# Optimization experiments

Measured on AMD Instinct MI355X. Metric: run time of the kernel, lower is better.

Reference implementation:

```python
import jax, jax.numpy as jnp
import numpy as np

N = 200000
NNZ = 6400000
E = 500000
IN_P, IN_F, IN_N = 62, 37, 37
HID, LAT, DEC_HID = 256, 128, 64


def _p(key, shape, scale=0.05):
    return scale * jax.random.normal(key, shape, dtype=jnp.float32)


def setup_inputs() -> dict:
    key = jax.random.key(0)
    ks = jax.random.split(key, 32)
    inp = {
        'x_process': jax.random.normal(ks[0], (N, IN_P), dtype=jnp.float32),
        'x_file': jax.random.normal(ks[1], (N, IN_F), dtype=jnp.float32),
        'x_network': jax.random.normal(ks[2], (N, IN_N), dtype=jnp.float32),
        'adj_rows': jax.random.randint(ks[3], (NNZ,), 0, N, dtype=jnp.int32),
        'adj_cols': jax.random.randint(ks[4], (NNZ,), 0, N, dtype=jnp.int32),
        'adj_vals': jax.random.uniform(ks[5], (NNZ,), dtype=jnp.float32) / 32.0,
        'edge_src': jax.random.randint(ks[6], (E,), 0, N, dtype=jnp.int32),
        'edge_dst': jax.random.randint(ks[7], (E,), 0, N, dtype=jnp.int32),
        # per-view encoder params (weights stored [in, out])
        'Wp1': _p(ks[8], (IN_P, HID)), 'bp1': jnp.zeros((HID,), jnp.float32),
        'Wp2': _p(ks[9], (HID, LAT)), 'bp2': jnp.zeros((LAT,), jnp.float32),
        'Wf1': _p(ks[10], (IN_F, HID)), 'bf1': jnp.zeros((HID,), jnp.float32),
        'Wf2': _p(ks[11], (HID, LAT)), 'bf2': jnp.zeros((LAT,), jnp.float32),
        'Wn1': _p(ks[12], (IN_N, HID)), 'bn1': jnp.zeros((HID,), jnp.float32),
        'Wn2': _p(ks[13], (HID, LAT)), 'bn2': jnp.zeros((LAT,), jnp.float32),
        # gates
        'Wgp': _p(ks[14], (LAT, 1)), 'bgp': jnp.zeros((1,), jnp.float32),
        'Wgf': _p(ks[15], (LAT, 1)), 'bgf': jnp.zeros((1,), jnp.float32),
        'Wgn': _p(ks[16], (LAT, 1)), 'bgn': jnp.zeros((1,), jnp.float32),
        # mlp edge decoder
        'Wd1': _p(ks[17], (4 * LAT, DEC_HID)), 'bd1': jnp.zeros((DEC_HID,), jnp.float32),
        'Wd2': _p(ks[18], (DEC_HID, 1)), 'bd2': jnp.zeros((1,), jnp.float32),
    }
    return inp


def _spmm(rows, cols, vals, x):
    # sparse (COO) adjacency @ dense x : gather cols, scale, scatter-add into rows
    return jax.ops.segment_sum(vals[:, None] * x[cols], rows, num_segments=N)


def _encode_view(x, rows, cols, vals, W1, b1, W2, b2):
    h = jax.nn.relu(_spmm(rows, cols, vals, x) @ W1 + b1)  # dropout=0 / eval mode
    return _spmm(rows, cols, vals, h) @ W2 + b2


def reference(x_process, x_file, x_network, adj_rows, adj_cols, adj_vals,
              edge_src, edge_dst,
              Wp1, bp1, Wp2, bp2, Wf1, bf1, Wf2, bf2, Wn1, bn1, Wn2, bn2,
              Wgp, bgp, Wgf, bgf, Wgn, bgn, Wd1, bd1, Wd2, bd2):
    zp = _encode_view(x_process, adj_rows, adj_cols, adj_vals, Wp1, bp1, Wp2, bp2)
    zf = _encode_view(x_file, adj_rows, adj_cols, adj_vals, Wf1, bf1, Wf2, bf2)
    zn = _encode_view(x_network, adj_rows, adj_cols, adj_vals, Wn1, bn1, Wn2, bn2)
    # multi-view softmax gating -> fused latent [N, LAT]
    scores = jnp.concatenate([zp @ Wgp + bgp, zf @ Wgf + bgf, zn @ Wgn + bgn], axis=1)
    alpha = jax.nn.softmax(scores, axis=1)
    z = alpha[:, 0:1] * zp + alpha[:, 1:2] * zf + alpha[:, 2:3] * zn
    # mlp edge decoder: gather src/dst, concat features, small MLP
    zs, zd = z[edge_src], z[edge_dst]
    feats = jnp.concatenate([zs, zd, zs * zd, jnp.abs(zs - zd)], axis=1)  # [E, 4*LAT]
    logits = jax.nn.relu(feats @ Wd1 + bd1) @ Wd2 + bd2
    return logits[:, 0]
```

## Files before the change

kernel.cpp:

```cpp
#include <hip/hip_runtime.h>
#include <math.h>

#define Nn 200000
#define NNZV 6400000
#define NE 500000
#define HID 256
#define LAT 128

typedef _Float16 h2 __attribute__((ext_vector_type(2)));
typedef _Float16 f16x4 __attribute__((ext_vector_type(4)));
typedef _Float16 f16x8 __attribute__((ext_vector_type(8)));
typedef float f32x4 __attribute__((ext_vector_type(4)));
typedef short s16x8 __attribute__((ext_vector_type(8)));
struct alignas(8) H4 { _Float16 h[4]; };

__device__ __forceinline__ float rdlanef(float v, int k){
  return __uint_as_float(__builtin_amdgcn_readlane(__float_as_uint(v), k));
}

__global__ __launch_bounds__(256) void k_zero(int* __restrict__ cnt){
  int i = blockIdx.x*256 + threadIdx.x;
  if(i < Nn) cnt[i] = 0;
}

__global__ __launch_bounds__(256) void k_count(const int* __restrict__ rows, int* __restrict__ cnt){
  int i = blockIdx.x*256 + threadIdx.x;
  if(i < NNZV) atomicAdd(&cnt[rows[i]], 1);
}

__global__ __launch_bounds__(512) void k_scan_block(const int* __restrict__ cnt, int* __restrict__ incl, int* __restrict__ bsum){
  __shared__ int s[512];
  int t = threadIdx.x;
  int i = blockIdx.x*512 + t;
  int v = (i < Nn) ? cnt[i] : 0;
  s[t] = v; __syncthreads();
  for(int off = 1; off < 512; off <<= 1){
    int x = (t >= off) ? s[t-off] : 0;
    __syncthreads();
    s[t] += x;
    __syncthreads();
  }
  if(i < Nn) incl[i] = s[t];
  if(t == 511) bsum[blockIdx.x] = s[t];
}

__global__ __launch_bounds__(512) void k_scan_bsum(int* __restrict__ bsum, int nb){
  __shared__ int s[512];
  int t = threadIdx.x;
  int v = (t < nb) ? bsum[t] : 0;
  s[t] = v; __syncthreads();
  for(int off = 1; off < 512; off <<= 1){
    int x = (t >= off) ? s[t-off] : 0;
    __syncthreads();
    s[t] += x;
    __syncthreads();
  }
  if(t < nb) bsum[t] = s[t] - v;
}

__global__ __launch_bounds__(256) void k_finish(const int* __restrict__ incl, const int* __restrict__ boff,
                                                int* __restrict__ row_ptr, int* __restrict__ cur){
  int i = blockIdx.x*256 + threadIdx.x;
  if(i < Nn){
    int v = incl[i] + boff[i >> 9];
    row_ptr[i+1] = v;
    if(i < Nn-1) cur[i+1] = v;
  }
  if(i == 0){ row_ptr[0] = 0; cur[0] = 0; }
}

__global__ __launch_bounds__(256) void k_scatter(const int* __restrict__ rows, const int* __restrict__ cols,
    const float* __restrict__ vals, int* __restrict__ cur,
    int* __restrict__ cols_s, _Float16* __restrict__ vals_s){
  int i = blockIdx.x*256 + threadIdx.x;
  if(i >= NNZV) return;
  int r = rows[i];
  int j = atomicAdd(&cur[r], 1);
  cols_s[j] = cols[i];
  vals_s[j] = (_Float16)vals[i];
}

__global__ __launch_bounds__(256) void k_xpack(const float* __restrict__ xp, const float* __restrict__ xf,
    const float* __restrict__ xn, _Float16* __restrict__ xc0, _Float16* __restrict__ xtl){
  int idx = blockIdx.x*256 + threadIdx.x;
  int row = idx/18, c8 = idx - row*18;
  if(row >= Nn) return;
  H4 ha, hb;
  #pragma unroll
  for(int q = 0; q < 8; q++){
    int c = c8*8 + q;
    float x;
    if(c < 62)       x = xp[row*62 + c];
    else if(c < 99)  x = xf[row*37 + (c-62)];
    else if(c == 99) x = 0.f;
    else if(c < 137) x = xn[row*37 + (c-100)];
    else             x = 0.f;
    if(q < 4) ha.h[q] = (_Float16)x; else hb.h[q-4] = (_Float16)x;
  }
  if(c8 < 16){
    *(H4*)&xc0[(size_t)row*128 + c8*8]     = ha;
    *(H4*)&xc0[(size_t)row*128 + c8*8 + 4] = hb;
  } else {
    int t = (c8-16)*8;
    *(H4*)&xtl[(size_t)row*16 + t]     = ha;
    *(H4*)&xtl[(size_t)row*16 + t + 4] = hb;
  }
}

__global__ __launch_bounds__(256) void k_wpackF(
    const float* __restrict__ Wp1, const float* __restrict__ Wf1, const float* __restrict__ Wn1,
    const float* __restrict__ Wp2, const float* __restrict__ Wf2, const float* __restrict__ Wn2,
    _Float16* __restrict__ w1fp, _Float16* __restrict__ w1ff, _Float16* __restrict__ w1fn,
    _Float16* __restrict__ w2fp, _Float16* __restrict__ w2ff, _Float16* __restrict__ w2fn){
  int i = blockIdx.x*256 + threadIdx.x;
  if(i >= 18432) return;
  int v = i / 6144, rem = i - v*6144;
  const float* W1 = (v==0)?Wp1:((v==1)?Wf1:Wn1);
  const float* W2 = (v==0)?Wp2:((v==1)?Wf2:Wn2);
  _Float16* d1 = (v==0)?w1fp:((v==1)?w1ff:w1fn);
  _Float16* d2 = (v==0)?w2fp:((v==1)?w2ff:w2fn);
  int Kv = (v==0)?62:37;
  f16x8 o;
  if(rem < 2048){
    int kt = rem >> 10, r2 = rem & 1023;
    int nt = r2 >> 6, l = r2 & 63;
    int krow = kt*32 + (l>>4)*8, col = nt*16 + (l&15);
    #pragma unroll
    for(int j = 0; j < 8; j++){
      int k = krow + j;
      o[j] = (k < Kv) ? (_Float16)W1[k*256 + col] : (_Float16)0.f;
    }
    *(f16x8*)&d1[rem*8] = o;
  } else {
    int r = rem - 2048;
    int kt = r >> 9, nt = (r >> 6) & 7, l = r & 63;
    int krow = kt*32 + (l>>4)*8, col = nt*16 + (l&15);
    #pragma unroll
    for(int j = 0; j < 8; j++)
      o[j] = (_Float16)W2[(krow + j)*128 + col];
    *(f16x8*)&d2[r*8] = o;
  }
}

__global__ void k_wg2(const float* __restrict__ Wp2, const float* __restrict__ Wgp,
                      const float* __restrict__ Wf2, const float* __restrict__ Wgf,
                      const float* __restrict__ Wn2, const float* __restrict__ Wgn,
                      float* __restrict__ wg2){
  int k = threadIdx.x;
  float p = 0.f, f = 0.f, n = 0.f;
  for(int c = 0; c < 128; c++){
    p = fmaf(Wp2[k*128 + c], Wgp[c], p);
    f = fmaf(Wf2[k*128 + c], Wgf[c], f);
    n = fmaf(Wn2[k*128 + c], Wgn[c], n);
  }
  wg2[k] = p; wg2[256 + k] = f; wg2[512 + k] = n;
}

__global__ void k_const(const float* b2p, const float* Wgp, const float* bgp,
                        const float* b2f, const float* Wgf, const float* bgf,
                        const float* b2n, const float* Wgn, const float* bgn,
                        float* c3){
  int l = threadIdx.x;
  float p = 0.f, f = 0.f, n = 0.f;
  for(int j = l; j < LAT; j += 64){
    p += b2p[j]*Wgp[j];
    f += b2f[j]*Wgf[j];
    n += b2n[j]*Wgn[j];
  }
  #pragma unroll
  for(int off = 32; off >= 1; off >>= 1){
    p += __shfl_xor(p, off);
    f += __shfl_xor(f, off);
    n += __shfl_xor(n, off);
  }
  if(l == 0){ c3[0] = p + bgp[0]; c3[1] = f + bgf[0]; c3[2] = n + bgn[0]; }
}

__device__ __forceinline__ void encode_view(
    int tid, int row0, int voff, int Kv, int vidx,
    const _Float16 (*sT)[152], _Float16 (*sTv)[72], _Float16 (*hT)[264],
    const _Float16* __restrict__ w1frag, const float* __restrict__ b1,
    const _Float16* __restrict__ w2frag, const float* __restrict__ wg2v,
    _Float16* __restrict__ Y3, float* __restrict__ yg4f){
  int w = tid >> 6, l = tid & 63;
  int kg = l >> 4, er = l & 15;
  int mrow = (w & 1)*16 + er;

  {
    int row = tid >> 3, c0 = (tid & 7)*8;
    f16x8 vv;
    #pragma unroll
    for(int q = 0; q < 8; q++){
      int c = c0 + q;
      vv[q] = (c < Kv) ? sT[row][voff + c] : (_Float16)0.f;
    }
    *(f16x8*)&sTv[row][c0] = vv;
  }
  __syncthreads();

  {
    f16x8 a0 = *(const f16x8*)&sTv[mrow][kg*8];
    f16x8 a1 = *(const f16x8*)&sTv[mrow][32 + kg*8];
    int ntb = (w >> 1)*8;
    #pragma unroll
    for(int nt8 = 0; nt8 < 8; nt8++){
      int nt = ntb + nt8;
      f16x8 b0 = *(const f16x8*)&w1frag[(size_t)((0*16 + nt)*64 + l)*8];
      f16x8 b1v = *(const f16x8*)&w1frag[(size_t)((1*16 + nt)*64 + l)*8];
      f32x4 acc = {0.f, 0.f, 0.f, 0.f};
      acc = __builtin_amdgcn_mfma_f32_16x16x32_f16(a0, b0, acc, 0, 0, 0);
      acc = __builtin_amdgcn_mfma_f32_16x16x32_f16(a1, b1v, acc, 0, 0, 0);
      int col = nt*16 + er;
      float bb = b1[col];
      #pragma unroll
      for(int j = 0; j < 4; j++)
        hT[(w & 1)*16 + kg*4 + j][col] = (_Float16)fmaxf(acc[j] + bb, 0.f);
    }
  }
  __syncthreads();

  {
    int row = tid >> 3, cg = tid & 7;
    float p = 0.f;
    #pragma unroll 8
    for(int kk = 0; kk < 32; kk++)
      p = fmaf((float)hT[row][cg*32 + kk], wg2v[cg*32 + kk], p);
    p += __shfl_xor(p, 1);
    p += __shfl_xor(p, 2);
    p += __shfl_xor(p, 4);
    if((tid & 7) == 0) yg4f[(size_t)(row0 + row)*4 + vidx] = p;
  }

  {
    f16x8 af[8];
    #pragma unroll
    for(int kt = 0; kt < 8; kt++)
      af[kt] = *(const f16x8*)&hT[mrow][kt*32 + kg*8];
    __syncthreads();
    _Float16* yst = &hT[0][0];
    int ntb = (w >> 1)*4;
    #pragma unroll
    for(int nt4 = 0; nt4 < 4; nt4++){
      int nt = ntb + nt4;
      f32x4 acc = {0.f, 0.f, 0.f, 0.f};
      #pragma unroll
      for(int kt = 0; kt < 8; kt++){
        f16x8 bf = *(const f16x8*)&w2frag[(size_t)((kt*8 + nt)*64 + l)*8];
        acc = __builtin_amdgcn_mfma_f32_16x16x32_f16(af[kt], bf, acc, 0, 0, 0);
      }
      int col = nt*16 + er;
      #pragma unroll
      for(int j = 0; j < 4; j++)
        yst[((w & 1)*16 + kg*4 + j)*132 + col] = (_Float16)acc[j];
    }
    __syncthreads();
    int row = tid >> 3, c0 = (tid & 7)*16;
    f16x8 y0 = *(const f16x8*)&yst[row*132 + c0];
    f16x8 y1 = *(const f16x8*)&yst[row*132 + c0 + 8];
    _Float16* yo = &Y3[(size_t)(row0 + row)*384 + vidx*128 + c0];
    *(f16x8*)yo       = y0;
    *(f16x8*)(yo + 8) = y1;
  }
  __syncthreads();
}

__global__ __launch_bounds__(256, 5) void k_encfused(
    const int* __restrict__ row_ptr, const int* __restrict__ cols_s, const _Float16* __restrict__ vals_s,
    const _Float16* __restrict__ xc0, const _Float16* __restrict__ xtl,
    const _Float16* __restrict__ w1fp, const float* __restrict__ bp1, const _Float16* __restrict__ w2fp,
    const _Float16* __restrict__ w1ff, const float* __restrict__ bf1, const _Float16* __restrict__ w2ff,
    const _Float16* __restrict__ w1fn, const float* __restrict__ bn1, const _Float16* __restrict__ w2fn,
    const float* __restrict__ wg2,
    _Float16* __restrict__ Y3, float* __restrict__ yg4f){
  __shared__ _Float16 sT[32][152];
  __shared__ _Float16 sTv[32][72];
  __shared__ _Float16 hT[32][264];
  int tid = threadIdx.x;
  int lane = tid & 63, wid = tid >> 6;
  int hl = lane & 31;
  int half = lane >> 5;
  int base = lane & 32;
  int row0 = blockIdx.x * 32;
  bool hast = (hl < 4);
  const char* xc0b = (const char*)xc0;
  const char* xtlb = (const char*)xtl;

  for(int p = 0; p < 4; p++){
    int rr = wid*8 + p*2 + half;
    int r = row0 + rr;
    int start = row_ptr[r], end = row_ptr[r+1];
    int len = end - start;
    int lenO = __shfl(len, lane ^ 32);
    int lenmax = len > lenO ? len : lenO;
    float a0 = 0.f, a1 = 0.f, a2 = 0.f, a3 = 0.f;
    float t0 = 0.f, t1 = 0.f, t2 = 0.f, t3 = 0.f;
    for(int j0 = 0; j0 < lenmax; j0 += 32){
      int m = len - j0; if(m > 32) m = 32; if(m < 0) m = 0;
      int mO = lenO - j0; if(mO > 32) mO = 32; if(mO < 0) mO = 0;
      int mmax = m > mO ? m : mO;
      int mycol = 0; float myval = 0.f;
      if(hl < m){
        mycol = cols_s[start + j0 + hl];
        myval = (float)vals_s[start + j0 + hl];
      }
      int mpad = (mmax + 3) & ~3;
      for(int k = 0; k < mpad; k += 4){
        #pragma unroll
        for(int q = 0; q < 4; q++){
          int c = __shfl(mycol, base + k + q);
          float v = __shfl(myval, base + k + q);
          f16x4 xa = *(const f16x4*)(xc0b + (((unsigned)c) << 8) + hl*8);
          a0 = fmaf((float)xa[0], v, a0);
          a1 = fmaf((float)xa[1], v, a1);
          a2 = fmaf((float)xa[2], v, a2);
          a3 = fmaf((float)xa[3], v, a3);
          if(hast){
            f16x4 xb = *(const f16x4*)(xtlb + ((unsigned)c)*32u + hl*8);
            t0 = fmaf((float)xb[0], v, t0);
            t1 = fmaf((float)xb[1], v, t1);
            t2 = fmaf((float)xb[2], v, t2);
            t3 = fmaf((float)xb[3], v, t3);
          }
        }
      }
    }
    h2 s01; s01[0] = (_Float16)a0; s01[1] = (_Float16)a1;
    h2 s23; s23[0] = (_Float16)a2; s23[1] = (_Float16)a3;
    *(h2*)&sT[rr][4*hl]     = s01;
    *(h2*)&sT[rr][4*hl + 2] = s23;
    if(hast){
      h2 u01; u01[0] = (_Float16)t0; u01[1] = (_Float16)t1;
      h2 u23; u23[0] = (_Float16)t2; u23[1] = (_Float16)t3;
      *(h2*)&sT[rr][128 + 4*hl]     = u01;
      *(h2*)&sT[rr][128 + 4*hl + 2] = u23;
    }
  }
  __syncthreads();

  encode_view(tid, row0, 0,   62, 0, sT, sTv, hT, w1fp, bp1, w2fp, wg2,       Y3, yg4f);
  encode_view(tid, row0, 62,  37, 1, sT, sTv, hT, w1ff, bf1, w2ff, wg2 + 256, Y3, yg4f);
  encode_view(tid, row0, 100, 37, 2, sT, sTv, hT, w1fn, bn1, w2fn, wg2 + 512, Y3, yg4f);
}

__global__ __launch_bounds__(256, 8) void k_spmm2f(
    const int* __restrict__ row_ptr, const int* __restrict__ cols_s, const _Float16* __restrict__ vals_s,
    const _Float16* __restrict__ Y3,
    const float4* __restrict__ yg4, const float* __restrict__ c3,
    const float* __restrict__ b2p, const float* __restrict__ b2f, const float* __restrict__ b2n,
    _Float16* __restrict__ z){
  int tid = threadIdx.x;
  int lane = tid & 63;
  int hl = lane & 31;
  int half = lane >> 5;
  int base = lane & 32;
  int r = blockIdx.x*8 + (tid >> 6)*2 + half;
  int start = row_ptr[r], end = row_ptr[r+1];
  int len = end - start;
  int lenO = __shfl(len, lane ^ 32);
  int lenmax = len > lenO ? len : lenO;
  unsigned lo = hl*8;
  float ap0=0.f, ap1=0.f, ap2=0.f, ap3=0.f;
  float af0=0.f, af1=0.f, af2=0.f, af3=0.f;
  float an0=0.f, an1=0.f, an2=0.f, an3=0.f;
  float scp=0.f, scf=0.f, scn=0.f;
  const char* Yb = (const char*)Y3;
  for(int j0 = 0; j0 < lenmax; j0 += 32){
    int m = len - j0; if(m > 32) m = 32; if(m < 0) m = 0;
    int mO = lenO - j0; if(mO > 32) mO = 32; if(mO < 0) mO = 0;
    int mmax = m > mO ? m : mO;
    int mycol = 0; float myval = 0.f;
    if(hl < m){
      mycol = cols_s[start + j0 + hl];
      myval = (float)vals_s[start + j0 + hl];
      float4 g = yg4[mycol];
      scp = fmaf(myval, g.x, scp);
      scf = fmaf(myval, g.y, scf);
      scn = fmaf(myval, g.z, scn);
    }
    int mpad = (mmax + 3) & ~3;
    for(int k = 0; k < mpad; k += 4){
      #pragma unroll
      for(int q = 0; q < 4; q++){
        int c = __shfl(mycol, base + k + q);
        float v = __shfl(myval, base + k + q);
        const char* p = Yb + ((unsigned)c)*768u + lo;
        f16x4 yp = *(const f16x4*)(p);
        f16x4 yf = *(const f16x4*)(p + 256);
        f16x4 yn = *(const f16x4*)(p + 512);
        ap0 = fmaf((float)yp[0], v, ap0); ap1 = fmaf((float)yp[1], v, ap1);
        ap2 = fmaf((float)yp[2], v, ap2); ap3 = fmaf((float)yp[3], v, ap3);
        af0 = fmaf((float)yf[0], v, af0); af1 = fmaf((float)yf[1], v, af1);
        af2 = fmaf((float)yf[2], v, af2); af3 = fmaf((float)yf[3], v, af3);
        an0 = fmaf((float)yn[0], v, an0); an1 = fmaf((float)yn[1], v, an1);
        an2 = fmaf((float)yn[2], v, an2); an3 = fmaf((float)yn[3], v, an3);
      }
    }
  }
  #pragma unroll
  for(int off = 16; off >= 1; off >>= 1){
    scp += __shfl_xor(scp, off);
    scf += __shfl_xor(scf, off);
    scn += __shfl_xor(scn, off);
  }
  float sp = scp + c3[0], sf = scf + c3[1], sn = scn + c3[2];
  float mx = fmaxf(sp, fmaxf(sf, sn));
  float ep = expf(sp - mx), ef = expf(sf - mx), en = expf(sn - mx);
  float inv = 1.f / (ep + ef + en);
  float A0 = ep*inv, A1 = ef*inv, A2 = en*inv;
  int o = hl*4;
  float4 bp = *(const float4*)&b2p[o];
  float4 bf = *(const float4*)&b2f[o];
  float4 bn = *(const float4*)&b2n[o];
  H4 uz;
  uz.h[0] = (_Float16)(A0*(ap0 + bp.x) + A1*(af0 + bf.x) + A2*(an0 + bn.x));
  uz.h[1] = (_Float16)(A0*(ap1 + bp.y) + A1*(af1 + bf.y) + A2*(an1 + bn.y));
  uz.h[2] = (_Float16)(A0*(ap2 + bp.z) + A1*(af2 + bf.z) + A2*(an2 + bn.z));
  uz.h[3] = (_Float16)(A0*(ap3 + bp.w) + A1*(af3 + bf.w) + A2*(an3 + bn.w));
  *(H4*)&z[(size_t)r*LAT + o] = uz;
}

#define DEC_TILES (NE/16)
__global__ __launch_bounds__(256) void k_dec(
    const _Float16* __restrict__ z, const int* __restrict__ esrc, const int* __restrict__ edst,
    const float* __restrict__ Wd1, const float* __restrict__ bd1,
    const float* __restrict__ Wd2, const float* __restrict__ bd2, float* __restrict__ out){
  __shared__ float part[4][16][68];
  int tid = threadIdx.x;
  int w  = tid >> 6;
  int l  = tid & 63;
  int erow = l & 15;
  int kg   = l >> 4;

  f16x8 bfr[4][4];
  #pragma unroll
  for(int kt = 0; kt < 4; kt++){
    #pragma unroll
    for(int nt = 0; nt < 4; nt++){
      f16x8 bb;
      #pragma unroll
      for(int j = 0; j < 8; j++)
        bb[j] = (_Float16)Wd1[(w*128 + kt*32 + kg*8 + j)*64 + nt*16 + erow];
      bfr[kt][nt] = bb;
    }
  }

  int n0 = (tid & 15) * 4;
  int e2 = tid >> 4;
  float4 bb1 = *(const float4*)&bd1[n0];
  float4 w2v = *(const float4*)&Wd2[n0];
  float bias2 = bd2[0];

  for(int tile = blockIdx.x; tile < DEC_TILES; tile += gridDim.x){
    int e = tile*16 + erow;
    int si = esrc[e], di = edst[e];
    const f16x8* zs = (const f16x8*)&z[(size_t)si*LAT];
    const f16x8* zd = (const f16x8*)&z[(size_t)di*LAT];
    f16x8 afr[4];
    if(w == 0){
      #pragma unroll
      for(int kt = 0; kt < 4; kt++) afr[kt] = zs[kt*4 + kg];
    } else if(w == 1){
      #pragma unroll
      for(int kt = 0; kt < 4; kt++) afr[kt] = zd[kt*4 + kg];
    } else if(w == 2){
      #pragma unroll
      for(int kt = 0; kt < 4; kt++) afr[kt] = zs[kt*4 + kg] * zd[kt*4 + kg];
    } else {
      #pragma unroll
      for(int kt = 0; kt < 4; kt++){
        f16x8 d = zs[kt*4 + kg] - zd[kt*4 + kg];
        s16x8 m = __builtin_bit_cast(s16x8, d) & (short)0x7fff;
        afr[kt] = __builtin_bit_cast(f16x8, m);
      }
    }
    f32x4 zero = {0.f, 0.f, 0.f, 0.f};
    f32x4 acc[4] = {zero, zero, zero, zero};
    #pragma unroll
    for(int kt = 0; kt < 4; kt++){
      #pragma unroll
      for(int nt = 0; nt < 4; nt++)
        acc[nt] = __builtin_amdgcn_mfma_f32_16x16x32_f16(afr[kt], bfr[kt][nt], acc[nt], 0, 0, 0);
    }
    #pragma unroll
    for(int nt = 0; nt < 4; nt++){
      #pragma unroll
      for(int j = 0; j < 4; j++)
        part[w][kg*4 + j][nt*16 + erow] = acc[nt][j];
    }
    __syncthreads();
    float s0 = part[0][e2][n0+0] + part[1][e2][n0+0] + part[2][e2][n0+0] + part[3][e2][n0+0];
    float s1 = part[0][e2][n0+1] + part[1][e2][n0+1] + part[2][e2][n0+1] + part[3][e2][n0+1];
    float s2 = part[0][e2][n0+2] + part[1][e2][n0+2] + part[2][e2][n0+2] + part[3][e2][n0+2];
    float s3 = part[0][e2][n0+3] + part[1][e2][n0+3] + part[2][e2][n0+3] + part[3][e2][n0+3];
    float p = fmaxf(s0 + bb1.x, 0.f)*w2v.x + fmaxf(s1 + bb1.y, 0.f)*w2v.y
            + fmaxf(s2 + bb1.z, 0.f)*w2v.z + fmaxf(s3 + bb1.w, 0.f)*w2v.w;
    #pragma unroll
    for(int off = 1; off < 16; off <<= 1) p += __shfl_xor(p, off);
    if((tid & 15) == 0) out[tile*16 + e2] = p + bias2;
    __syncthreads();
  }
}

extern "C" void kernel_launch(void* const* d_in, const int* in_sizes, int n_in,
                              void* d_out, int out_size, void* d_ws, size_t ws_size,
                              hipStream_t stream) {
  const float* xp  = (const float*)d_in[0];
  const float* xf  = (const float*)d_in[1];
  const float* xn  = (const float*)d_in[2];
  const int* arows = (const int*)d_in[3];
  const int* acols = (const int*)d_in[4];
  const float* avals = (const float*)d_in[5];
  const int* esrc  = (const int*)d_in[6];
  const int* edst  = (const int*)d_in[7];
  const float* Wp1 = (const float*)d_in[8];  const float* bp1 = (const float*)d_in[9];
  const float* Wp2 = (const float*)d_in[10]; const float* bp2 = (const float*)d_in[11];
  const float* Wf1 = (const float*)d_in[12]; const float* bf1 = (const float*)d_in[13];
  const float* Wf2 = (const float*)d_in[14]; const float* bf2w = (const float*)d_in[15];
  const float* Wn1 = (const float*)d_in[16]; const float* bn1 = (const float*)d_in[17];
  const float* Wn2 = (const float*)d_in[18]; const float* bn2 = (const float*)d_in[19];
  const float* Wgp = (const float*)d_in[20]; const float* bgp = (const float*)d_in[21];
  const float* Wgf = (const float*)d_in[22]; const float* bgf = (const float*)d_in[23];
  const float* Wgn = (const float*)d_in[24]; const float* bgn = (const float*)d_in[25];
  const float* Wd1 = (const float*)d_in[26]; const float* bd1 = (const float*)d_in[27];
  const float* Wd2 = (const float*)d_in[28]; const float* bd2 = (const float*)d_in[29];
  float* out = (float*)d_out;
  (void)in_sizes; (void)n_in; (void)out_size; (void)ws_size;

  char* base = (char*)d_ws;
  size_t off = 0;
  auto alloc = [&](size_t nbytes) -> char* {
    off = (off + 255) & ~(size_t)255;
    char* p = base + off;
    off += nbytes;
    return p;
  };
  int*      row_ptr = (int*)     alloc((size_t)(Nn + 1) * 4);
  int*      cols_s  = (int*)     alloc((size_t)NNZV * 4);
  _Float16* vals_s  = (_Float16*)alloc((size_t)NNZV * 2);
  _Float16* xcat0   = (_Float16*)alloc((size_t)Nn * 128 * 2);
  _Float16* xtail   = (_Float16*)alloc((size_t)Nn * 16 * 2);
  _Float16* Y3      = (_Float16*)alloc((size_t)Nn * 384 * 2);
  float*    yg4     = (float*)   alloc((size_t)Nn * 4 * 4);
  float*    c3      = (float*)   alloc(256);
  float*    wg2     = (float*)   alloc(3 * 256 * 4);
  _Float16* w1fp = (_Float16*)alloc(16384*2);
  _Float16* w1ff = (_Float16*)alloc(16384*2);
  _Float16* w1fn = (_Float16*)alloc(16384*2);
  _Float16* w2fp = (_Float16*)alloc(32768*2);
  _Float16* w2ff = (_Float16*)alloc(32768*2);
  _Float16* w2fn = (_Float16*)alloc(32768*2);
  _Float16* z = xcat0;
  int* cur  = (int*)((char*)xcat0);
  int* incl = (int*)((char*)xcat0 + 1000000);
  int* bsum = (int*)((char*)xcat0 + 2000000);

  int NB = (Nn + 511) / 512;

  k_zero   <<<(Nn + 255)/256, 256, 0, stream>>>(cur);
  k_count  <<<(NNZV + 255)/256, 256, 0, stream>>>(arows, cur);
  k_scan_block<<<NB, 512, 0, stream>>>(cur, incl, bsum);
  k_scan_bsum<<<1, 512, 0, stream>>>(bsum, NB);
  k_finish <<<(Nn + 255)/256, 256, 0, stream>>>(incl, bsum, row_ptr, cur);
  k_scatter<<<(NNZV + 255)/256, 256, 0, stream>>>(arows, acols, avals, cur, cols_s, vals_s);

  k_xpack<<<(Nn*18 + 255)/256, 256, 0, stream>>>(xp, xf, xn, xcat0, xtail);
  k_wpackF<<<72, 256, 0, stream>>>(Wp1, Wf1, Wn1, Wp2, Wf2, Wn2,
                                   w1fp, w1ff, w1fn, w2fp, w2ff, w2fn);
  k_wg2<<<1, 256, 0, stream>>>(Wp2, Wgp, Wf2, Wgf, Wn2, Wgn, wg2);
  k_const<<<1, 64, 0, stream>>>(bp2, Wgp, bgp, bf2w, Wgf, bgf, bn2, Wgn, bgn, c3);

  k_encfused<<<Nn/32, 256, 0, stream>>>(row_ptr, cols_s, vals_s, xcat0, xtail,
      w1fp, bp1, w2fp,  w1ff, bf1, w2ff,  w1fn, bn1, w2fn,  wg2,
      Y3, yg4);

  k_spmm2f<<<Nn/8, 256, 0, stream>>>(row_ptr, cols_s, vals_s, Y3,
      (const float4*)yg4, c3, bp2, bf2w, bn2, z);

  k_dec<<<2048, 256, 0, stream>>>(z, esrc, edst, Wd1, bd1, Wd2, bd2, out);
}
```

Baseline: 2.308 ms.

## Split second SpMM into score kernel and two column-half gather passes

Moves the gating-score accumulation and softmax out of the second SpMM into a separate k_score kernel that writes per-row alpha into the reused xtail buffer. The SpMM itself is split into two launches, each handling half of the 128 latent columns with 4-byte loads per view, so each pass touches a smaller slice of Y3 and may get better cache locality from the random column gathers. In exchange, the CSR indices and values are read three times, there are extra launches, and each gather is narrower per lane.

Result: no change. 2.296 ms (-0.5%).

```diff
diff --git a/kernel.cpp b/kernel.cpp
--- a/kernel.cpp
+++ b/kernel.cpp
@@ -13,10 +13,6 @@
 typedef float f32x4 __attribute__((ext_vector_type(4)));
 typedef short s16x8 __attribute__((ext_vector_type(8)));
 struct alignas(8) H4 { _Float16 h[4]; };
-
-__device__ __forceinline__ float rdlanef(float v, int k){
-  return __uint_as_float(__builtin_amdgcn_readlane(__float_as_uint(v), k));
-}
 
 __global__ __launch_bounds__(256) void k_zero(int* __restrict__ cnt){
   int i = blockIdx.x*256 + threadIdx.x;
@@ -342,10 +338,45 @@
   encode_view(tid, row0, 100, 37, 2, sT, sTv, hT, w1fn, bn1, w2fn, wg2 + 512, Y3, yg4f);
 }
 
-__global__ __launch_bounds__(256, 8) void k_spmm2f(
+__global__ __launch_bounds__(256, 8) void k_score(
     const int* __restrict__ row_ptr, const int* __restrict__ cols_s, const _Float16* __restrict__ vals_s,
-    const _Float16* __restrict__ Y3,
     const float4* __restrict__ yg4, const float* __restrict__ c3,
+    float4* __restrict__ alpha){
+  int tid = threadIdx.x;
+  int lane = tid & 63;
+  int hl = lane & 31;
+  int half = lane >> 5;
+  int r = blockIdx.x*8 + (tid >> 6)*2 + half;
+  int start = row_ptr[r], end = row_ptr[r+1];
+  int len = end - start;
+  float scp = 0.f, scf = 0.f, scn = 0.f;
+  for(int j0 = hl; j0 < len; j0 += 32){
+    int c = cols_s[start + j0];
+    float v = (float)vals_s[start + j0];
+    float4 g = yg4[c];
+    scp = fmaf(v, g.x, scp);
+    scf = fmaf(v, g.y, scf);
+    scn = fmaf(v, g.z, scn);
+  }
+  #pragma unroll
+  for(int off = 16; off >= 1; off >>= 1){
+    scp += __shfl_xor(scp, off);
+    scf += __shfl_xor(scf, off);
+    scn += __shfl_xor(scn, off);
+  }
+  if(hl == 0){
+    float sp = scp + c3[0], sf = scf + c3[1], sn = scn + c3[2];
+    float mx = fmaxf(sp, fmaxf(sf, sn));
+    float ep = expf(sp - mx), ef = expf(sf - mx), en = expf(sn - mx);
+    float inv = 1.f / (ep + ef + en);
+    alpha[r] = make_float4(ep*inv, ef*inv, en*inv, 0.f);
+  }
+}
+
+template<int H>
+__global__ __launch_bounds__(256, 8) void k_spmm2h(
+    const int* __restrict__ row_ptr, const int* __restrict__ cols_s, const _Float16* __restrict__ vals_s,
+    const _Float16* __restrict__ Y3, const float4* __restrict__ alpha,
     const float* __restrict__ b2p, const float* __restrict__ b2f, const float* __restrict__ b2n,
     _Float16* __restrict__ z){
   int tid = threadIdx.x;
@@ -358,11 +389,8 @@
   int len = end - start;
   int lenO = __shfl(len, lane ^ 32);
   int lenmax = len > lenO ? len : lenO;
-  unsigned lo = hl*8;
-  float ap0=0.f, ap1=0.f, ap2=0.f, ap3=0.f;
-  float af0=0.f, af1=0.f, af2=0.f, af3=0.f;
-  float an0=0.f, an1=0.f, an2=0.f, an3=0.f;
-  float scp=0.f, scf=0.f, scn=0.f;
+  unsigned lo = H*128 + hl*4;
+  float ap0=0.f, ap1=0.f, af0=0.f, af1=0.f, an0=0.f, an1=0.f;
   const char* Yb = (const char*)Y3;
   for(int j0 = 0; j0 < lenmax; j0 += 32){
     int m = len - j0; if(m > 32) m = 32; if(m < 0) m = 0;
@@ -372,10 +400,6 @@
     if(hl < m){
       mycol = cols_s[start + j0 + hl];
       myval = (float)vals_s[start + j0 + hl];
-      float4 g = yg4[mycol];
-      scp = fmaf(myval, g.x, scp);
-      scf = fmaf(myval, g.y, scf);
-      scn = fmaf(myval, g.z, scn);
     }
     int mpad = (mmax + 3) & ~3;
     for(int k = 0; k < mpad; k += 4){
@@ -384,39 +408,24 @@
         int c = __shfl(mycol, base + k + q);
         float v = __shfl(myval, base + k + q);
         const char* p = Yb + ((unsigned)c)*768u + lo;
-        f16x4 yp = *(const f16x4*)(p);
-        f16x4 yf = *(const f16x4*)(p + 256);
-        f16x4 yn = *(const f16x4*)(p + 512);
+        h2 yp = *(const h2*)(p);
+        h2 yf = *(const h2*)(p + 256);
+        h2 yn = *(const h2*)(p + 512);
         ap0 = fmaf((float)yp[0], v, ap0); ap1 = fmaf((float)yp[1], v, ap1);
-        ap2 = fmaf((float)yp[2], v, ap2); ap3 = fmaf((float)yp[3], v, ap3);
         af0 = fmaf((float)yf[0], v, af0); af1 = fmaf((float)yf[1], v, af1);
-        af2 = fmaf((float)yf[2], v, af2); af3 = fmaf((float)yf[3], v, af3);
         an0 = fmaf((float)yn[0], v, an0); an1 = fmaf((float)yn[1], v, an1);
-        an2 = fmaf((float)yn[2], v, an2); an3 = fmaf((float)yn[3], v, an3);
       }
     }
   }
-  #pragma unroll
-  for(int off = 16; off >= 1; off >>= 1){
-    scp += __shfl_xor(scp, off);
-    scf += __shfl_xor(scf, off);
-    scn += __shfl_xor(scn, off);
-  }
-  float sp = scp + c3[0], sf = scf + c3[1], sn = scn + c3[2];
-  float mx = fmaxf(sp, fmaxf(sf, sn));
-  float ep = expf(sp - mx), ef = expf(sf - mx), en = expf(sn - mx);
-  float inv = 1.f / (ep + ef + en);
-  float A0 = ep*inv, A1 = ef*inv, A2 = en*inv;
-  int o = hl*4;
-  float4 bp = *(const float4*)&b2p[o];
-  float4 bf = *(const float4*)&b2f[o];
-  float4 bn = *(const float4*)&b2n[o];
-  H4 uz;
-  uz.h[0] = (_Float16)(A0*(ap0 + bp.x) + A1*(af0 + bf.x) + A2*(an0 + bn.x));
-  uz.h[1] = (_Float16)(A0*(ap1 + bp.y) + A1*(af1 + bf.y) + A2*(an1 + bn.y));
-  uz.h[2] = (_Float16)(A0*(ap2 + bp.z) + A1*(af2 + bf.z) + A2*(an2 + bn.z));
-  uz.h[3] = (_Float16)(A0*(ap3 + bp.w) + A1*(af3 + bf.w) + A2*(an3 + bn.w));
-  *(H4*)&z[(size_t)r*LAT + o] = uz;
+  float4 al = alpha[r];
+  int o = H*64 + hl*2;
+  float2 bp = *(const float2*)&b2p[o];
+  float2 bf = *(const float2*)&b2f[o];
+  float2 bn = *(const float2*)&b2n[o];
+  float z0 = al.x*(ap0 + bp.x) + al.y*(af0 + bf.x) + al.z*(an0 + bn.x);
+  float z1 = al.x*(ap1 + bp.y) + al.y*(af1 + bf.y) + al.z*(an1 + bn.y);
+  h2 uz; uz[0] = (_Float16)z0; uz[1] = (_Float16)z1;
+  *(h2*)&z[(size_t)r*LAT + o] = uz;
 }
 
 #define DEC_TILES (NE/16)
@@ -549,7 +558,8 @@
   _Float16* w2fp = (_Float16*)alloc(32768*2);
   _Float16* w2ff = (_Float16*)alloc(32768*2);
   _Float16* w2fn = (_Float16*)alloc(32768*2);
-  _Float16* z = xcat0;
+  _Float16* z     = xcat0;
+  float4*   alpha = (float4*)xtail;
   int* cur  = (int*)((char*)xcat0);
   int* incl = (int*)((char*)xcat0 + 1000000);
   int* bsum = (int*)((char*)xcat0 + 2000000);
@@ -573,8 +583,13 @@
       w1fp, bp1, w2fp,  w1ff, bf1, w2ff,  w1fn, bn1, w2fn,  wg2,
       Y3, yg4);
 
-  k_spmm2f<<<Nn/8, 256, 0, stream>>>(row_ptr, cols_s, vals_s, Y3,
-      (const float4*)yg4, c3, bp2, bf2w, bn2, z);
+  k_score<<<Nn/8, 256, 0, stream>>>(row_ptr, cols_s, vals_s,
+      (const float4*)yg4, c3, alpha);
+
+  k_spmm2h<0><<<Nn/8, 256, 0, stream>>>(row_ptr, cols_s, vals_s, Y3, alpha,
+      bp2, bf2w, bn2, z);
+  k_spmm2h<1><<<Nn/8, 256, 0, stream>>>(row_ptr, cols_s, vals_s, Y3, alpha,
+      bp2, bf2w, bn2, z);
 
   k_dec<<<2048, 256, 0, stream>>>(z, esrc, edst, Wd1, bd1, Wd2, bd2, out);
 }
```
